# Performance work log

Hardware: AMD Instinct MI355X
Metric: run time of the kernel (lower is better)

The kernel has to match this reference:

```python
import jax, jax.numpy as jnp
from jax import lax
import numpy as np

DN = ('NCHW', 'OIHW', 'NCHW')


def conv(x, w, b, pad=0):
    y = lax.conv_general_dilated(x, w, (1, 1), [(pad, pad), (pad, pad)],
                                 dimension_numbers=DN)
    return y + b[None, :, None, None]


def deconv(x, w, b, stride=1):
    # PyTorch ConvTranspose2d weight is (in, out, kH, kW); equivalent conv uses
    # flipped, in/out-transposed kernel with lhs dilation = stride, pad = k-1.
    k = w.shape[2]
    wt = jnp.flip(w, (2, 3)).transpose(1, 0, 2, 3)
    y = lax.conv_general_dilated(x, wt, (1, 1), [(k - 1, k - 1), (k - 1, k - 1)],
                                 lhs_dilation=(stride, stride), dimension_numbers=DN)
    return y + b[None, :, None, None]


def maxpool2(x):
    return lax.reduce_window(x, -jnp.inf, lax.max, (1, 1, 2, 2), (1, 1, 2, 2), 'VALID')


def setup_inputs() -> dict:
    key = jax.random.key(0)
    ks = jax.random.split(key, 12)
    B = 256

    def he(k, shape, fan_in):
        return jax.random.normal(k, shape, jnp.float32) * np.sqrt(2.0 / fan_in)

    inp = {
        'x': jax.random.normal(ks[0], (B, 1, 28, 28), jnp.float32),
        # encoder convs
        'w1': he(ks[1], (128, 1, 5, 5), 1 * 25), 'b1': jnp.zeros((128,), jnp.float32),
        'w2': he(ks[2], (128, 128, 5, 5), 128 * 25), 'b2': jnp.zeros((128,), jnp.float32),
        'w3': he(ks[3], (128, 128, 5, 5), 128 * 25), 'b3': jnp.zeros((128,), jnp.float32),
        # decoder transposed convs (torch shape: in, out, kH, kW)
        't1w': he(ks[4], (128, 128, 4, 4), 128 * 16), 't1b': jnp.zeros((128,), jnp.float32),
        't2w': he(ks[5], (128, 128, 4, 4), 128 * 16), 't2b': jnp.zeros((128,), jnp.float32),
        't3w': he(ks[6], (128, 128, 5, 5), 128 * 25), 't3b': jnp.zeros((128,), jnp.float32),
        't4w': he(ks[7], (128, 128, 5, 5), 128 * 25), 't4b': jnp.zeros((128,), jnp.float32),
        # mu_net 1x1 conv
        'mw': he(ks[8], (1, 128, 1, 1), 128), 'mb': jnp.zeros((1,), jnp.float32),
        # codebook: Embedding(128, 128), init ~ N(0, 1)
        'dict_w': jax.random.normal(ks[9], (128, 128), jnp.float32),
    }
    return inp


def reference(x, w1, b1, w2, b2, w3, b3,
              t1w, t1b, t2w, t2b, t3w, t3b, t4w, t4b,
              mw, mb, dict_w):
    BETA, RATE = 0.25, 5.0
    # ---- encoder ----
    h = jax.nn.relu(conv(x, w1, b1, pad=0))          # (B,128,24,24)
    h = jax.nn.relu(conv(h, w2, b2, pad=2))          # (B,128,24,24)
    h = maxpool2(h)                                  # (B,128,12,12)
    h = conv(h, w3, b3, pad=2)                       # (B,128,12,12)
    z = maxpool2(h)                                  # (B,128,6,6)

    # ---- nearest_neighbor (faithful: argmax of distance, as in the source) ----
    z_sg = lax.stop_gradient(z)
    z2 = jnp.sum(z_sg * z_sg, axis=1, keepdims=True)          # (B,1,6,6)
    w2n = jnp.sum(dict_w * dict_w, axis=1)                     # (K,)
    cross = jnp.einsum('bchw,kc->bkhw', z_sg, lax.stop_gradient(dict_w))
    d2 = z2 + w2n[None, :, None, None] - 2.0 * cross           # (B,K,6,6)
    index = jnp.argmax(d2, axis=1)                             # (B,6,6) int

    # ---- embedding gather ----
    val = dict_w[index].transpose(0, 3, 1, 2)                  # (B,128,6,6)

    # ---- decoder on detached codes ----
    f = lax.stop_gradient(val)
    f = jax.nn.relu(deconv(f, t1w, t1b, stride=1))             # (B,128,9,9)
    f = jax.nn.relu(deconv(f, t2w, t2b, stride=2))             # (B,128,20,20)
    f = jax.nn.relu(deconv(f, t3w, t3b, stride=1))             # (B,128,24,24)
    f = jax.nn.relu(deconv(f, t4w, t4b, stride=1))             # (B,128,28,28)
    mu = conv(f, mw, mb, pad=0)                                # (B,1,28,28)

    loss_rec = jnp.mean((mu - x) ** 2)
    dict_loss = jnp.mean((val - lax.stop_gradient(z)) ** 2) * RATE
    enc_loss = jnp.mean((z - lax.stop_gradient(val)) ** 2) * BETA * RATE
    var_loss = jnp.zeros((), jnp.float32)
    losses = jnp.stack([loss_rec, dict_loss, enc_loss, var_loss])
    return losses, index
```

## Files before the change

kernel.cpp:

```cpp
#include <hip/hip_runtime.h>
#include <hip/hip_bf16.h>


#define B_ 256

typedef __attribute__((ext_vector_type(8))) short s16x8;
typedef __attribute__((ext_vector_type(4))) short s16x4;
typedef __attribute__((ext_vector_type(8))) _Float16 f16x8;
typedef __attribute__((ext_vector_type(4))) float f32x4;

__device__ inline ushort f2bf(float f) {
  union { __hip_bfloat16 h; ushort u; } cv;
  cv.h = __float2bfloat16(f);
  return cv.u;
}

__global__ __launch_bounds__(256) void prep_all(
    const float* __restrict__ t1w, const float* __restrict__ t3w,
    const float* __restrict__ t4w, const float* __restrict__ t2w,
    const float* __restrict__ w2, const float* __restrict__ w3,
    ushort* __restrict__ wp1, ushort* __restrict__ wp3,
    ushort* __restrict__ wp4, ushort* __restrict__ wp2,
    _Float16* __restrict__ w2h, _Float16* __restrict__ w2l,
    _Float16* __restrict__ w3h, _Float16* __restrict__ w3l) {
  const int b = blockIdx.x, t = threadIdx.x;
  if (b < 1024) {
    int idx = b * 256 + t;
    int ci = idx & 127, co = (idx >> 7) & 127, tap = idx >> 14;
    wp1[idx] = f2bf(t1w[((size_t)ci * 128 + co) * 16 + (15 - tap)]);
  } else if (b < 2624) {
    int idx = (b - 1024) * 256 + t;
    int ci = idx & 127, co = (idx >> 7) & 127, tap = idx >> 14;
    wp3[idx] = f2bf(t3w[((size_t)ci * 128 + co) * 25 + (24 - tap)]);
  } else if (b < 4224) {
    int idx = (b - 2624) * 256 + t;
    int ci = idx & 127, co = (idx >> 7) & 127, tap = idx >> 14;
    wp4[idx] = f2bf(t4w[((size_t)ci * 128 + co) * 25 + (24 - tap)]);
  } else if (b < 5248) {
    int idx = (b - 4224) * 256 + t;
    int ci = idx & 127, co = (idx >> 7) & 127;
    int tap = (idx >> 14) & 3, pp = idx >> 16;
    int u = tap >> 1, v = tap & 1, py = pp >> 1, px = pp & 1;
    wp2[idx] = f2bf(
        t2w[(((size_t)ci * 128 + co) * 4 + (py + 2 * u)) * 4 + (px + 2 * v)]);
  } else if (b < 6848) {
    int idx = (b - 5248) * 256 + t;
    int ci = idx & 127, co = (idx >> 7) & 127, tap = idx >> 14;
    float v = w2[((size_t)co * 128 + ci) * 25 + tap];
    _Float16 h = (_Float16)v;
    w2h[idx] = h;
    w2l[idx] = (_Float16)(v - (float)h);
  } else {
    int idx = (b - 6848) * 256 + t;
    int ci = idx & 127, co = (idx >> 7) & 127, tap = idx >> 14;
    float v = w3[((size_t)co * 128 + ci) * 25 + tap];
    _Float16 h = (_Float16)v;
    w3h[idx] = h;
    w3l[idx] = (_Float16)(v - (float)h);
  }
}

__global__ __launch_bounds__(256) void conv1_kernel(
    const float* __restrict__ x, const float* __restrict__ w,
    const float* __restrict__ b, _Float16* __restrict__ oh,
    _Float16* __restrict__ ol) {
  const int n = blockIdx.x;
  __shared__ float xl[784];
  __shared__ float wl[128 * 25];
  __shared__ float bl[128];
  const int t = threadIdx.x;
  for (int e = t; e < 784; e += 256) xl[e] = x[n * 784 + e];
  for (int e = t; e < 3200; e += 256) wl[e] = w[e];
  if (t < 128) bl[t] = b[t];
  __syncthreads();
  const size_t nb = (size_t)n * 73728;
  for (int idx = t; idx < 73728; idx += 256) {
    int co = idx & 127, p = idx >> 7;
    int y = p / 24, xx = p % 24;
    float acc = bl[co];
    const float* wc = &wl[co * 25];
#pragma unroll
    for (int ky = 0; ky < 5; ky++)
#pragma unroll
      for (int kx = 0; kx < 5; kx++)
        acc += xl[(y + ky) * 28 + xx + kx] * wc[ky * 5 + kx];
    float v = fmaxf(acc, 0.f);
    _Float16 h = (_Float16)v;
    oh[nb + idx] = h;
    ol[nb + idx] = (_Float16)(v - (float)h);
  }
}

template <int IW, int K, int PAD, int TR, bool RELU, bool OUT_F32, int PWX>
__global__ __launch_bounds__(256, 3) void conv_mfma_pool(
    const _Float16* __restrict__ inh, const _Float16* __restrict__ inl,
    const _Float16* __restrict__ wph, const _Float16* __restrict__ wpl,
    const float* __restrict__ bias, _Float16* __restrict__ outh,
    _Float16* __restrict__ outl, float* __restrict__ outf) {
  constexpr int IH = IW, OW = IW, OH = IW;
  constexpr int PW = PWX;
  constexpr int SROWS = TR + K - 1;
  constexpr int S = SROWS * PW;
  constexpr int NPOS = TR * OW;
  constexpr int NCH = NPOS / 16;
  constexpr int SCRP = NPOS + 1;
  constexpr int K2 = K * K;
  constexpr int PITCH = 40;
  constexpr int LIN_ELT = S * PITCH;
  constexpr int LIN_BYTES = 2 * LIN_ELT * 2;
  constexpr int SCR_BYTES = 64 * SCRP * 4;
  constexpr int SMEM_BYTES = LIN_BYTES > SCR_BYTES ? LIN_BYTES : SCR_BYTES;
  static_assert(NPOS % 16 == 0, "");
  static_assert(TR % 2 == 0 && OW % 2 == 0, "");
  static_assert(PW >= OW + K - 1, "");
  __shared__ __align__(16) char smem[SMEM_BYTES];
  _Float16* linh = (_Float16*)smem;
  _Float16* linl = linh + LIN_ELT;
  const int n = blockIdx.x;
  const int r0 = blockIdx.y * TR;
  const int t = threadIdx.x;
  const int wv = t >> 6;
  const int lane = t & 63;
  const int nn = lane & 15;
  const int q = lane >> 4;
  f32x4 acc0[NCH], acc1[NCH];
  int boff[NCH];
#pragma unroll
  for (int c = 0; c < NCH; c++) {
    acc0[c] = f32x4{0.f, 0.f, 0.f, 0.f};
    acc1[c] = f32x4{0.f, 0.f, 0.f, 0.f};
    int p = c * 16 + nn;
    boff[c] = ((p / OW) * PW + (p % OW)) * PITCH + q * 8;
  }
  const int rowA = wv * 16 + nn;
  const int rowB = (wv + 4) * 16 + nn;
  for (int cb = 0; cb < 4; cb++) {
    const int ci0 = cb * 32;
    __syncthreads();
    for (int e = t; e < S * 4; e += 256) {
      int sp = e >> 2, j = e & 3;
      int r = sp / PW, c = sp - r * PW;
      int ir = r0 + r - PAD, ic = c - PAD;
      f16x8 vh = {0, 0, 0, 0, 0, 0, 0, 0};
      f16x8 vl = {0, 0, 0, 0, 0, 0, 0, 0};
      if (ir >= 0 && ir < IH && ic >= 0 && ic < IW) {
        size_t g = ((size_t)n * (IH * IW) + ir * IW + ic) * 128 + ci0 + j * 8;
        vh = *(const f16x8*)&inh[g];
        vl = *(const f16x8*)&inl[g];
      }
      int st = sp * PITCH + j * 8;
      *(f16x8*)&linh[st] = vh;
      *(f16x8*)&linl[st] = vl;
    }
    __syncthreads();
    const size_t gA = (size_t)rowA * 128 + ci0 + q * 8;
    const size_t gB = (size_t)rowB * 128 + ci0 + q * 8;
    f16x8 cah0 = *(const f16x8*)&wph[gA];
    f16x8 cal0 = *(const f16x8*)&wpl[gA];
    f16x8 cah1 = *(const f16x8*)&wph[gB];
    f16x8 cal1 = *(const f16x8*)&wpl[gB];
    for (int tap = 0; tap < K2; tap++) {
      f16x8 nah0 = cah0, nal0 = cal0, nah1 = cah1, nal1 = cal1;
      if (tap + 1 < K2) {
        size_t oA = gA + (size_t)(tap + 1) * 16384;
        size_t oB = gB + (size_t)(tap + 1) * 16384;
        nah0 = *(const f16x8*)&wph[oA];
        nal0 = *(const f16x8*)&wpl[oA];
        nah1 = *(const f16x8*)&wph[oB];
        nal1 = *(const f16x8*)&wpl[oB];
      }
      const int ky = tap / K, kx = tap - ky * K;
      const int tp = (ky * PW + kx) * PITCH;
#pragma unroll
      for (int c = 0; c < NCH; c++) {
        int off = boff[c] + tp;
        f16x8 bh = *(const f16x8*)&linh[off];
        f16x8 bl = *(const f16x8*)&linl[off];
        acc0[c] =
            __builtin_amdgcn_mfma_f32_16x16x32_f16(cah0, bh, acc0[c], 0, 0, 0);
        acc0[c] =
            __builtin_amdgcn_mfma_f32_16x16x32_f16(cah0, bl, acc0[c], 0, 0, 0);
        acc0[c] =
            __builtin_amdgcn_mfma_f32_16x16x32_f16(cal0, bh, acc0[c], 0, 0, 0);
        acc1[c] =
            __builtin_amdgcn_mfma_f32_16x16x32_f16(cah1, bh, acc1[c], 0, 0, 0);
        acc1[c] =
            __builtin_amdgcn_mfma_f32_16x16x32_f16(cah1, bl, acc1[c], 0, 0, 0);
        acc1[c] =
            __builtin_amdgcn_mfma_f32_16x16x32_f16(cal1, bh, acc1[c], 0, 0, 0);
      }
      cah0 = nah0; cal0 = nal0; cah1 = nah1; cal1 = nal1;
    }
  }
  __syncthreads();
  float* scr = (float*)smem + wv * 16 * SCRP;
#pragma unroll
  for (int j = 0; j < 2; j++) {
    const int cot = (j ? wv + 4 : wv) * 16;
#pragma unroll
    for (int c = 0; c < NCH; c++) {
      f32x4 a = j ? acc1[c] : acc0[c];
#pragma unroll
      for (int r = 0; r < 4; r++) {
        float v = a[r] + bias[cot + q * 4 + r];
        if (RELU) v = fmaxf(v, 0.f);
        scr[(q * 4 + r) * SCRP + c * 16 + nn] = v;
      }
    }
    __syncthreads();
    for (int e = lane; e < 16 * (TR / 2) * (OW / 2); e += 64) {
      int co_l = e & 15;
      int rem = e >> 4;
      int pr = rem / (OW / 2), pc = rem - pr * (OW / 2);
      const float* s = scr + co_l * SCRP;
      int lp = (2 * pr) * OW + 2 * pc;
      float m =
          fmaxf(fmaxf(s[lp], s[lp + 1]), fmaxf(s[lp + OW], s[lp + OW + 1]));
      int sp_out = (r0 / 2 + pr) * (OW / 2) + pc;
      size_t go =
          ((size_t)n * ((OH / 2) * (OW / 2)) + sp_out) * 128 + cot + co_l;
      if (OUT_F32) {
        outf[go] = m;
      } else {
        _Float16 h = (_Float16)m;
        outh[go] = h;
        outl[go] = (_Float16)(m - (float)h);
      }
    }
    __syncthreads();
  }
}

__global__ __launch_bounds__(256) void vq_kernel(
    const float* __restrict__ z, const float* __restrict__ dict,
    float* __restrict__ val, ushort* __restrict__ val_bf,
    float* __restrict__ out_idx) {
  const int n = blockIdx.x;
  __shared__ float zl[36 * 128];
  __shared__ float d2[36 * 129];
  __shared__ float w2n[128];
  __shared__ int bk[36];
  const int t = threadIdx.x;
  const float* zn = z + (size_t)n * 4608;
  for (int e = t; e < 4608; e += 256) zl[e] = zn[e];
  if (t < 128) {
    float s = 0.f;
    const float* wr = dict + t * 128;
    for (int c = 0; c < 128; c++) s += wr[c] * wr[c];
    w2n[t] = s;
  }
  __syncthreads();
  const int k = t & 127, pg = t >> 7;
  float dot[18];
#pragma unroll
  for (int i = 0; i < 18; i++) dot[i] = 0.f;
  const float* wr = dict + k * 128;
  for (int c = 0; c < 128; c++) {
    float wv = wr[c];
#pragma unroll
    for (int i = 0; i < 18; i++) dot[i] += zl[(pg * 18 + i) * 128 + c] * wv;
  }
  float wn = w2n[k];
#pragma unroll
  for (int i = 0; i < 18; i++) d2[(pg * 18 + i) * 129 + k] = wn - 2.f * dot[i];
  __syncthreads();
  if (t < 36) {
    const float* dr = &d2[t * 129];
    float best = dr[0];
    int bi = 0;
    for (int kk = 1; kk < 128; kk++) {
      float v = dr[kk];
      if (v > best) { best = v; bi = kk; }
    }
    bk[t] = bi;
    out_idx[n * 36 + t] = (float)bi;
  }
  __syncthreads();
  float* vn = val + (size_t)n * 4608;
  ushort* vbn = val_bf + (size_t)n * 4608;
  for (int e = t; e < 4608; e += 256) {
    int c = e & 127, p = e >> 7;
    float v = dict[bk[p] * 128 + c];
    vn[e] = v;
    vbn[e] = f2bf(v);
  }
}

template <int IH, int IW, int OH, int OW, int K, int TR, bool MU_FUSE, int PWX>
__global__ __launch_bounds__(256, 2) void deconv_mfma(
    const ushort* __restrict__ in, const ushort* __restrict__ wprep,
    const float* __restrict__ bias, const float* __restrict__ mw,
    void* __restrict__ outp) {
  constexpr int PAD = K - 1;
  constexpr int PW = PWX;
  constexpr int K2 = K * K;
  constexpr int SROWS = TR + K - 1;
  constexpr int S = SROWS * PW;
  constexpr int NPOS = TR * OW;
  constexpr int NCH = (NPOS + 15) / 16;
  constexpr int PITCH = 40;
  constexpr int LIN_ELT = S * PITCH;
  constexpr int NSTG = (S * 4 + 255) / 256;
  static_assert(PW >= OW + K - 1, "");
  __shared__ __align__(16) ushort lin[2][LIN_ELT];
  const int n = blockIdx.x;
  const int r0 = blockIdx.y * TR;
  const int t = threadIdx.x;
  const int wv = t >> 6;
  const int lane = t & 63;
  const int nn = lane & 15;
  const int q = lane >> 4;
  f32x4 acc0[NCH], acc1[NCH];
  int boff[NCH];
#pragma unroll
  for (int c = 0; c < NCH; c++) {
    acc0[c] = f32x4{0.f, 0.f, 0.f, 0.f};
    acc1[c] = f32x4{0.f, 0.f, 0.f, 0.f};
    int p = c * 16 + nn;
    int pc = p < NPOS ? p : NPOS - 1;
    boff[c] = ((pc / OW) * PW + (pc % OW)) * PITCH + q * 8;
  }
  s16x8 stg[NSTG];
  auto load_stage = [&](int ci0) {
#pragma unroll
    for (int i = 0; i < NSTG; i++) {
      int e = t + i * 256;
      s16x8 v = {0, 0, 0, 0, 0, 0, 0, 0};
      if (e < S * 4) {
        int sp = e >> 2, j = e & 3;
        int rr = sp / PW, cc = sp - rr * PW;
        int ir = r0 + rr - PAD, ic = cc - PAD;
        if (ir >= 0 && ir < IH && ic >= 0 && ic < IW)
          v = *(const s16x8*)&in[((size_t)n * (IH * IW) + ir * IW + ic) * 128 +
                                 ci0 + j * 8];
      }
      stg[i] = v;
    }
  };
  auto store_stage = [&](int bsel) {
#pragma unroll
    for (int i = 0; i < NSTG; i++) {
      int e = t + i * 256;
      if (e < S * 4) {
        int sp = e >> 2, j = e & 3;
        *(s16x8*)&lin[bsel][sp * PITCH + j * 8] = stg[i];
      }
    }
  };

  load_stage(0);
  store_stage(0);
  __syncthreads();
  for (int cb = 0; cb < 4; cb++) {
    const int ci0 = cb * 32;
    if (cb < 3) load_stage(ci0 + 32);
    const ushort* L = lin[cb & 1];
    const size_t gA = (size_t)(wv * 16 + nn) * 128 + ci0 + q * 8;
    const size_t gB = (size_t)((wv + 4) * 16 + nn) * 128 + ci0 + q * 8;
    s16x8 ca0 = *(const s16x8*)&wprep[gA];
    s16x8 ca1 = *(const s16x8*)&wprep[gB];
    for (int tap = 0; tap < K2; tap++) {
      s16x8 na0 = ca0, na1 = ca1;
      if (tap + 1 < K2) {
        na0 = *(const s16x8*)&wprep[gA + (size_t)(tap + 1) * 16384];
        na1 = *(const s16x8*)&wprep[gB + (size_t)(tap + 1) * 16384];
      }
      const int ky = tap / K, kx = tap - ky * K;
      const int tp = (ky * PW + kx) * PITCH;
#pragma unroll
      for (int c = 0; c < NCH; c++) {
        s16x8 b = *(const s16x8*)&L[boff[c] + tp];
        acc0[c] =
            __builtin_amdgcn_mfma_f32_16x16x32_bf16(ca0, b, acc0[c], 0, 0, 0);
        acc1[c] =
            __builtin_amdgcn_mfma_f32_16x16x32_bf16(ca1, b, acc1[c], 0, 0, 0);
      }
      ca0 = na0; ca1 = na1;
    }
    if (cb < 3) {
      store_stage((cb + 1) & 1);
      __syncthreads();
    }
  }
  const int co_a = wv * 16 + q * 4;
  const int co_b = (wv + 4) * 16 + q * 4;
  float ba[4], bb[4];
#pragma unroll
  for (int r = 0; r < 4; r++) {
    ba[r] = bias[co_a + r];
    bb[r] = bias[co_b + r];
  }
  if (!MU_FUSE) {
    ushort* out = (ushort*)outp;
#pragma unroll
    for (int c = 0; c < NCH; c++) {
      int p = c * 16 + nn;
      if (p < NPOS) {
        size_t go = ((size_t)n * (OH * OW) + r0 * OW + p) * 128;
        s16x4 pa, pb;
#pragma unroll
        for (int r = 0; r < 4; r++) {
          pa[r] = (short)f2bf(fmaxf(acc0[c][r] + ba[r], 0.f));
          pb[r] = (short)f2bf(fmaxf(acc1[c][r] + bb[r], 0.f));
        }
        *(s16x4*)&out[go + co_a] = pa;
        *(s16x4*)&out[go + co_b] = pb;
      }
    }
  } else {
    float* out = (float*)outp;
    float wa[4], wb[4];
#pragma unroll
    for (int r = 0; r < 4; r++) {
      wa[r] = mw[co_a + r];
      wb[r] = mw[co_b + r];
    }
#pragma unroll
    for (int c = 0; c < NCH; c++) {
      int p = c * 16 + nn;
      float s = 0.f;
#pragma unroll
      for (int r = 0; r < 4; r++) {
        s += fmaxf(acc0[c][r] + ba[r], 0.f) * wa[r];
        s += fmaxf(acc1[c][r] + bb[r], 0.f) * wb[r];
      }
      s += __shfl_xor(s, 16);
      s += __shfl_xor(s, 32);
      if (q == 0 && p < NPOS)
        atomicAdd(&out[(size_t)n * (OH * OW) + r0 * OW + p], s);
    }
  }
}

__global__ __launch_bounds__(256, 3) void deconv_s2_mfma(
    const ushort* __restrict__ in, const ushort* __restrict__ wp2,
    const float* __restrict__ bias, ushort* __restrict__ out) {
  constexpr int NCH = 7;
  constexpr int PITCH = 40;
  constexpr int PW = 18;
  constexpr int S = 11 * PW;
  const int n = blockIdx.x;
  const int pp = blockIdx.y;
  const int py = pp >> 1, px = pp & 1;
  __shared__ __align__(16) ushort lin[S * PITCH];
  const int t = threadIdx.x;
  const int wv = t >> 6;
  const int lane = t & 63;
  const int nn = lane & 15;
  const int q = lane >> 4;
  f32x4 acc0[NCH], acc1[NCH];
  int boff[NCH];
#pragma unroll
  for (int c = 0; c < NCH; c++) {
    acc0[c] = f32x4{0.f, 0.f, 0.f, 0.f};
    acc1[c] = f32x4{0.f, 0.f, 0.f, 0.f};
    int p = c * 16 + nn;
    int pc = p < 100 ? p : 99;
    boff[c] = ((pc / 10) * PW + (pc % 10)) * PITCH + q * 8;
  }
  const int toffs[4] = {PW + 1, PW, 1, 0};
  for (int cb = 0; cb < 4; cb++) {
    const int ci0 = cb * 32;
    __syncthreads();
    for (int e = t; e < S * 4; e += 256) {
      int sp = e >> 2, j = e & 3;
      int r = sp / PW, c2 = sp - r * PW;
      int ir = r - 1, ic = c2 - 1;
      s16x8 v = {0, 0, 0, 0, 0, 0, 0, 0};
      if (ir >= 0 && ir < 9 && ic >= 0 && ic < 9)
        v = *(const s16x8*)&in[((size_t)n * 81 + ir * 9 + ic) * 128 + ci0 +
                               j * 8];
      *(s16x8*)&lin[sp * PITCH + j * 8] = v;
    }
    __syncthreads();
    const size_t gA =
        ((size_t)(pp * 4) * 128 + wv * 16 + nn) * 128 + ci0 + q * 8;
    const size_t gB =
        ((size_t)(pp * 4) * 128 + (wv + 4) * 16 + nn) * 128 + ci0 + q * 8;
    s16x8 ca0 = *(const s16x8*)&wp2[gA];
    s16x8 ca1 = *(const s16x8*)&wp2[gB];
    for (int tap = 0; tap < 4; tap++) {
      s16x8 na0 = ca0, na1 = ca1;
      if (tap + 1 < 4) {
        na0 = *(const s16x8*)&wp2[gA + (size_t)(tap + 1) * 16384];
        na1 = *(const s16x8*)&wp2[gB + (size_t)(tap + 1) * 16384];
      }
      const int tp = toffs[tap] * PITCH;
#pragma unroll
      for (int c = 0; c < NCH; c++) {
        s16x8 b = *(const s16x8*)&lin[boff[c] + tp];
        acc0[c] =
            __builtin_amdgcn_mfma_f32_16x16x32_bf16(ca0, b, acc0[c], 0, 0, 0);
        acc1[c] =
            __builtin_amdgcn_mfma_f32_16x16x32_bf16(ca1, b, acc1[c], 0, 0, 0);
      }
      ca0 = na0; ca1 = na1;
    }
  }
  const int co_a = wv * 16 + q * 4;
  const int co_b = (wv + 4) * 16 + q * 4;
#pragma unroll
  for (int c = 0; c < NCH; c++) {
    int p = c * 16 + nn;
    if (p < 100) {
      int oy = 2 * (p / 10) + py, ox = 2 * (p % 10) + px;
      size_t go = ((size_t)n * 400 + oy * 20 + ox) * 128;
      s16x4 pa, pb;
#pragma unroll
      for (int r = 0; r < 4; r++) {
        pa[r] = (short)f2bf(fmaxf(acc0[c][r] + bias[co_a + r], 0.f));
        pb[r] = (short)f2bf(fmaxf(acc1[c][r] + bias[co_b + r], 0.f));
      }
      *(s16x4*)&out[go + co_a] = pa;
      *(s16x4*)&out[go + co_b] = pb;
    }
  }
}

__global__ __launch_bounds__(256) void loss_kernel(
    const float* __restrict__ mu, const float* __restrict__ mb,
    const float* __restrict__ x, const float4* __restrict__ val4,
    const float4* __restrict__ z4, float* __restrict__ out) {
  const int b = blockIdx.x, t = threadIdx.x;
  __shared__ float red[256];
  if (b < 784) {
    int i = b * 256 + t;
    float d = mu[i] + mb[0] - x[i];
    red[t] = d * d;
  } else {
    int i = (b - 784) * 256 + t;
    float4 a = val4[i], zz = z4[i];
    float dx = a.x - zz.x, dy = a.y - zz.y, dz = a.z - zz.z, dw = a.w - zz.w;
    red[t] = dx * dx + dy * dy + dz * dz + dw * dw;
  }
  __syncthreads();
  for (int off = 128; off > 0; off >>= 1) {
    if (t < off) red[t] += red[t + off];
    __syncthreads();
  }
  if (t == 0) {
    if (b < 784) {
      atomicAdd(out, red[0] * (1.0f / 200704.f));
    } else {
      atomicAdd(out + 1, red[0] * (5.f / 1179648.f));
      atomicAdd(out + 2, red[0] * (1.25f / 1179648.f));
    }
  }
}

extern "C" void kernel_launch(void* const* d_in, const int* in_sizes, int n_in,
                              void* d_out, int out_size, void* d_ws,
                              size_t ws_size, hipStream_t stream) {
  const float* x = (const float*)d_in[0];
  const float* w1 = (const float*)d_in[1];
  const float* b1 = (const float*)d_in[2];
  const float* w2 = (const float*)d_in[3];
  const float* b2 = (const float*)d_in[4];
  const float* w3 = (const float*)d_in[5];
  const float* b3 = (const float*)d_in[6];
  const float* t1w = (const float*)d_in[7];
  const float* t1b = (const float*)d_in[8];
  const float* t2w = (const float*)d_in[9];
  const float* t2b = (const float*)d_in[10];
  const float* t3w = (const float*)d_in[11];
  const float* t3b = (const float*)d_in[12];
  const float* t4w = (const float*)d_in[13];
  const float* t4b = (const float*)d_in[14];
  const float* mw = (const float*)d_in[15];
  const float* mb = (const float*)d_in[16];
  const float* dictw = (const float*)d_in[17];
  float* out = (float*)d_out;

  float* p = (float*)d_ws;
  _Float16* h1h = (_Float16*)p; p += 9437184;
  _Float16* h1l = (_Float16*)p; p += 9437184;
  _Float16* p1h = (_Float16*)p; p += 2359296;
  _Float16* p1l = (_Float16*)p; p += 2359296;
  float* z = p; p += 1179648;
  float* val = p; p += 1179648;
  ushort* val_bf = (ushort*)p; p += 589824;
  float* mu = p; p += 200704;
  ushort* wp1 = (ushort*)p; p += 131072;
  ushort* wp3 = (ushort*)p; p += 204800;
  ushort* wp4 = (ushort*)p; p += 204800;
  ushort* wp2 = (ushort*)p; p += 131072;
  _Float16* w2h = (_Float16*)p; p += 204800;
  _Float16* w2l = (_Float16*)p; p += 204800;
  _Float16* w3h = (_Float16*)p; p += 204800;
  _Float16* w3l = (_Float16*)p; p += 204800;
  ushort* f1 = (ushort*)p1h;
  ushort* f2 = (ushort*)h1l;
  ushort* f3 = (ushort*)h1h;

  hipMemsetAsync(d_out, 0, 4 * sizeof(float), stream);
  hipMemsetAsync(mu, 0, 200704 * sizeof(float), stream);

  prep_all<<<8448, 256, 0, stream>>>(t1w, t3w, t4w, t2w, w2, w3, wp1, wp3, wp4,
                                     wp2, w2h, w2l, w3h, w3l);

  conv1_kernel<<<B_, 256, 0, stream>>>(x, w1, b1, h1h, h1l);
  conv_mfma_pool<24, 5, 2, 6, true, false, 28>
      <<<dim3(B_, 4), 256, 0, stream>>>(h1h, h1l, w2h, w2l, b2, p1h, p1l,
                                        nullptr);
  conv_mfma_pool<12, 5, 2, 4, false, true, 20>
      <<<dim3(B_, 3), 256, 0, stream>>>(p1h, p1l, w3h, w3l, b3, nullptr,
                                        nullptr, z);
  vq_kernel<<<B_, 256, 0, stream>>>(z, dictw, val, val_bf, out + 4);
  deconv_mfma<6, 6, 9, 9, 4, 9, false, 17>
      <<<dim3(B_, 1), 256, 0, stream>>>(val_bf, wp1, t1b, nullptr, f1);
  deconv_s2_mfma<<<dim3(B_, 4), 256, 0, stream>>>(f1, wp2, t2b, f2);
  deconv_mfma<20, 20, 24, 24, 5, 8, false, 28>
      <<<dim3(B_, 3), 256, 0, stream>>>(f2, wp3, t3b, nullptr, f3);
  deconv_mfma<24, 24, 28, 28, 5, 7, true, 36>
      <<<dim3(B_, 4), 256, 0, stream>>>(f3, wp4, t4b, mw, mu);
  loss_kernel<<<1936, 256, 0, stream>>>(mu, mb, x, (const float4*)val,
                                        (const float4*)z, out);
}
```

Measured before the change: 913.3 us.

## Specialize conv2 with register-blocked MFMA tiles and double-buffered weight prefetch

Replaces the generic templated conv2+pool kernel with a dedicated kernel. Each wave holds a 5x4 block of 16x16 accumulators, covering 64 output channels by up to 80 positions, so each LDS B-fragment feeds four MFMA groups. Weight fragments for the next tap are prefetched from global into registers, and the next channel chunk of input is staged through registers while the current one computes. The larger accumulator footprint lowers occupancy to two blocks per CU, and the pooling epilogue runs in four passes through a shared scratch buffer.

```diff
diff --git a/kernel.cpp b/kernel.cpp
--- a/kernel.cpp
+++ b/kernel.cpp
@@ -91,6 +91,164 @@
   }
 }
 
+__global__ __launch_bounds__(256, 2) void conv2_mfma_pool(
+    const _Float16* __restrict__ inh, const _Float16* __restrict__ inl,
+    const _Float16* __restrict__ wph, const _Float16* __restrict__ wpl,
+    const float* __restrict__ bias, _Float16* __restrict__ outh,
+    _Float16* __restrict__ outl) {
+  constexpr int PW = 28;
+  constexpr int S = 10 * PW;
+  constexpr int NPOS = 144;
+  constexpr int SCRP = NPOS + 1;
+  constexpr int PITCH = 40;
+  constexpr int LIN_ELT = S * PITCH;
+  __shared__ __align__(16) char smem[2 * LIN_ELT * 2];
+  _Float16* linh = (_Float16*)smem;
+  _Float16* linl = linh + LIN_ELT;
+  const int n = blockIdx.x;
+  const int r0 = blockIdx.y * 6;
+  const int t = threadIdx.x;
+  const int wv = t >> 6;
+  const int lane = t & 63;
+  const int nn = lane & 15;
+  const int q = lane >> 4;
+  const int pairid = wv >> 1;
+  const int coset = wv & 1;
+  f32x4 acc[5][4];
+#pragma unroll
+  for (int cL = 0; cL < 5; cL++)
+#pragma unroll
+    for (int g = 0; g < 4; g++) acc[cL][g] = f32x4{0.f, 0.f, 0.f, 0.f};
+  int boff[5];
+#pragma unroll
+  for (int cL = 0; cL < 5; cL++) {
+    int cg = pairid ? 5 + cL : cL;
+    int p = cg * 16 + nn;
+    boff[cL] = ((p / 24) * PW + (p % 24)) * PITCH + q * 8;
+  }
+  size_t gA[4];
+#pragma unroll
+  for (int g = 0; g < 4; g++)
+    gA[g] = (size_t)(coset * 64 + g * 16 + nn) * 128 + q * 8;
+
+  f16x8 stgh[5], stgl[5];
+  auto load_stage = [&](int ci0) {
+#pragma unroll
+    for (int i = 0; i < 5; i++) {
+      int e = t + i * 256;
+      f16x8 vh = {0, 0, 0, 0, 0, 0, 0, 0};
+      f16x8 vl = {0, 0, 0, 0, 0, 0, 0, 0};
+      if (e < S * 4) {
+        int sp = e >> 2, j = e & 3;
+        int r = sp / PW, c = sp - r * PW;
+        int ir = r0 + r - 2, ic = c - 2;
+        if (ir >= 0 && ir < 24 && ic >= 0 && ic < 24) {
+          size_t g2 = ((size_t)n * 576 + ir * 24 + ic) * 128 + ci0 + j * 8;
+          vh = *(const f16x8*)&inh[g2];
+          vl = *(const f16x8*)&inl[g2];
+        }
+      }
+      stgh[i] = vh;
+      stgl[i] = vl;
+    }
+  };
+  auto store_stage = [&]() {
+#pragma unroll
+    for (int i = 0; i < 5; i++) {
+      int e = t + i * 256;
+      if (e < S * 4) {
+        int sp = e >> 2, j = e & 3;
+        *(f16x8*)&linh[sp * PITCH + j * 8] = stgh[i];
+        *(f16x8*)&linl[sp * PITCH + j * 8] = stgl[i];
+      }
+    }
+  };
+
+  load_stage(0);
+  store_stage();
+  __syncthreads();
+  for (int cb = 0; cb < 4; cb++) {
+    const int ci0 = cb * 32;
+    f16x8 cah[4], cal[4];
+#pragma unroll
+    for (int g = 0; g < 4; g++) {
+      cah[g] = *(const f16x8*)&wph[gA[g] + ci0];
+      cal[g] = *(const f16x8*)&wpl[gA[g] + ci0];
+    }
+    if (cb < 3) load_stage(ci0 + 32);
+    for (int tap = 0; tap < 25; tap++) {
+      f16x8 nah[4], nal[4];
+#pragma unroll
+      for (int g = 0; g < 4; g++) { nah[g] = cah[g]; nal[g] = cal[g]; }
+      if (tap + 1 < 25) {
+        const size_t to = (size_t)(tap + 1) * 16384 + ci0;
+#pragma unroll
+        for (int g = 0; g < 4; g++) {
+          nah[g] = *(const f16x8*)&wph[gA[g] + to];
+          nal[g] = *(const f16x8*)&wpl[gA[g] + to];
+        }
+      }
+      const int ky = tap / 5, kx = tap - ky * 5;
+      const int tp = (ky * PW + kx) * PITCH;
+#pragma unroll
+      for (int cL = 0; cL < 5; cL++) {
+        if (pairid == 0 || cL < 4) {
+          f16x8 bh = *(const f16x8*)&linh[boff[cL] + tp];
+          f16x8 bl = *(const f16x8*)&linl[boff[cL] + tp];
+#pragma unroll
+          for (int g = 0; g < 4; g++) {
+            acc[cL][g] = __builtin_amdgcn_mfma_f32_16x16x32_f16(cah[g], bh,
+                                                               acc[cL][g], 0, 0, 0);
+            acc[cL][g] = __builtin_amdgcn_mfma_f32_16x16x32_f16(cah[g], bl,
+                                                               acc[cL][g], 0, 0, 0);
+            acc[cL][g] = __builtin_amdgcn_mfma_f32_16x16x32_f16(cal[g], bh,
+                                                               acc[cL][g], 0, 0, 0);
+          }
+        }
+      }
+#pragma unroll
+      for (int g = 0; g < 4; g++) { cah[g] = nah[g]; cal[g] = nal[g]; }
+    }
+    if (cb < 3) {
+      __syncthreads();
+      store_stage();
+      __syncthreads();
+    }
+  }
+  __syncthreads();
+  float* scr = (float*)smem;
+#pragma unroll
+  for (int g = 0; g < 4; g++) {
+#pragma unroll
+    for (int cL = 0; cL < 5; cL++) {
+      if (pairid == 0 || cL < 4) {
+        const int cg = pairid ? 5 + cL : cL;
+#pragma unroll
+        for (int r = 0; r < 4; r++) {
+          float v =
+              fmaxf(acc[cL][g][r] + bias[coset * 64 + g * 16 + q * 4 + r], 0.f);
+          scr[(coset * 16 + q * 4 + r) * SCRP + cg * 16 + nn] = v;
+        }
+      }
+    }
+    __syncthreads();
+    for (int e = t; e < 1152; e += 256) {
+      int co32 = e & 31, rem = e >> 5;
+      int pr = rem / 12, pc = rem - pr * 12;
+      const float* s = scr + co32 * SCRP;
+      int lp = (2 * pr) * 24 + 2 * pc;
+      float m =
+          fmaxf(fmaxf(s[lp], s[lp + 1]), fmaxf(s[lp + 24], s[lp + 25]));
+      int co_g = (co32 >> 4) * 64 + g * 16 + (co32 & 15);
+      size_t go = ((size_t)n * 144 + (size_t)(r0 / 2 + pr) * 12 + pc) * 128 + co_g;
+      _Float16 h = (_Float16)m;
+      outh[go] = h;
+      outl[go] = (_Float16)(m - (float)h);
+    }
+    __syncthreads();
+  }
+}
+
 template <int IW, int K, int PAD, int TR, bool RELU, bool OUT_F32, int PWX>
 __global__ __launch_bounds__(256, 3) void conv_mfma_pool(
     const _Float16* __restrict__ inh, const _Float16* __restrict__ inl,
@@ -599,9 +757,8 @@
                                      wp2, w2h, w2l, w3h, w3l);
 
   conv1_kernel<<<B_, 256, 0, stream>>>(x, w1, b1, h1h, h1l);
-  conv_mfma_pool<24, 5, 2, 6, true, false, 28>
-      <<<dim3(B_, 4), 256, 0, stream>>>(h1h, h1l, w2h, w2l, b2, p1h, p1l,
-                                        nullptr);
+  conv2_mfma_pool<<<dim3(B_, 4), 256, 0, stream>>>(h1h, h1l, w2h, w2l, b2,
+                                                   p1h, p1l);
   conv_mfma_pool<12, 5, 2, 4, false, true, 20>
       <<<dim3(B_, 3), 256, 0, stream>>>(p1h, p1l, w3h, w3l, b3, nullptr,
                                         nullptr, z);
```

Result: slower. 1.014 ms (+11.0%).

## Retile deconv MFMA warps into 64-channel by half-position tiles

Applied to the files above, without the earlier changes.

Each wave previously computed 32 output channels (two 16-row groups) across all position tiles. Now wave pairs split the position tiles and each wave covers 64 output channels (four groups), so each LDS B-fragment load feeds four MFMAs instead of two. This cuts LDS read traffic per MFMA, but each wave now issues twice as many weight loads per tap. The uneven split when NCH is odd also leaves the second pair of waves with less work.

```diff
diff --git a/kernel.cpp b/kernel.cpp
--- a/kernel.cpp
+++ b/kernel.cpp
@@ -287,7 +287,8 @@
 }
 
 template <int IH, int IW, int OH, int OW, int K, int TR, bool MU_FUSE, int PWX>
-__global__ __launch_bounds__(256, 2) void deconv_mfma(
+__global__ __attribute__((amdgpu_flat_work_group_size(256, 256),
+                          amdgpu_waves_per_eu(2, 2))) void deconv_mfma(
     const ushort* __restrict__ in, const ushort* __restrict__ wprep,
     const float* __restrict__ bias, const float* __restrict__ mw,
     void* __restrict__ outp) {
@@ -298,6 +299,8 @@
   constexpr int S = SROWS * PW;
   constexpr int NPOS = TR * OW;
   constexpr int NCH = (NPOS + 15) / 16;
+  constexpr int NT0 = (NCH + 1) / 2;
+  constexpr int NT1 = NCH - NT0;
   constexpr int PITCH = 40;
   constexpr int LIN_ELT = S * PITCH;
   constexpr int NSTG = (S * 4 + 255) / 256;
@@ -310,15 +313,19 @@
   const int lane = t & 63;
   const int nn = lane & 15;
   const int q = lane >> 4;
-  f32x4 acc0[NCH], acc1[NCH];
-  int boff[NCH];
-#pragma unroll
-  for (int c = 0; c < NCH; c++) {
-    acc0[c] = f32x4{0.f, 0.f, 0.f, 0.f};
-    acc1[c] = f32x4{0.f, 0.f, 0.f, 0.f};
-    int p = c * 16 + nn;
+  const int pairid = wv >> 1;
+  const int cohalf = wv & 1;
+  f32x4 acc[NT0][4];
+  int boff[NT0];
+#pragma unroll
+  for (int tL = 0; tL < NT0; tL++) {
+#pragma unroll
+    for (int g = 0; g < 4; g++) acc[tL][g] = f32x4{0.f, 0.f, 0.f, 0.f};
+    int tg = pairid * NT0 + tL;
+    if (tg > NCH - 1) tg = NCH - 1;
+    int p = tg * 16 + nn;
     int pc = p < NPOS ? p : NPOS - 1;
-    boff[c] = ((pc / OW) * PW + (pc % OW)) * PITCH + q * 8;
+    boff[tL] = ((pc / OW) * PW + (pc % OW)) * PITCH + q * 8;
   }
   s16x8 stg[NSTG];
   auto load_stage = [&](int ci0) {
@@ -355,79 +362,95 @@
     const int ci0 = cb * 32;
     if (cb < 3) load_stage(ci0 + 32);
     const ushort* L = lin[cb & 1];
-    const size_t gA = (size_t)(wv * 16 + nn) * 128 + ci0 + q * 8;
-    const size_t gB = (size_t)((wv + 4) * 16 + nn) * 128 + ci0 + q * 8;
-    s16x8 ca0 = *(const s16x8*)&wprep[gA];
-    s16x8 ca1 = *(const s16x8*)&wprep[gB];
+    size_t gA[4];
+#pragma unroll
+    for (int g = 0; g < 4; g++)
+      gA[g] = (size_t)(cohalf * 64 + g * 16 + nn) * 128 + ci0 + q * 8;
+    s16x8 ca[4];
+#pragma unroll
+    for (int g = 0; g < 4; g++) ca[g] = *(const s16x8*)&wprep[gA[g]];
     for (int tap = 0; tap < K2; tap++) {
-      s16x8 na0 = ca0, na1 = ca1;
+      s16x8 na[4];
+#pragma unroll
+      for (int g = 0; g < 4; g++) na[g] = ca[g];
       if (tap + 1 < K2) {
-        na0 = *(const s16x8*)&wprep[gA + (size_t)(tap + 1) * 16384];
-        na1 = *(const s16x8*)&wprep[gB + (size_t)(tap + 1) * 16384];
+        const size_t to = (size_t)(tap + 1) * 16384;
+#pragma unroll
+        for (int g = 0; g < 4; g++)
+          na[g] = *(const s16x8*)&wprep[gA[g] + to];
       }
       const int ky = tap / K, kx = tap - ky * K;
       const int tp = (ky * PW + kx) * PITCH;
 #pragma unroll
-      for (int c = 0; c < NCH; c++) {
-        s16x8 b = *(const s16x8*)&L[boff[c] + tp];
-        acc0[c] =
-            __builtin_amdgcn_mfma_f32_16x16x32_bf16(ca0, b, acc0[c], 0, 0, 0);
-        acc1[c] =
-            __builtin_amdgcn_mfma_f32_16x16x32_bf16(ca1, b, acc1[c], 0, 0, 0);
-      }
-      ca0 = na0; ca1 = na1;
+      for (int tL = 0; tL < NT0; tL++) {
+        if (pairid == 0 || tL < NT1) {
+          s16x8 b = *(const s16x8*)&L[boff[tL] + tp];
+#pragma unroll
+          for (int g = 0; g < 4; g++)
+            acc[tL][g] = __builtin_amdgcn_mfma_f32_16x16x32_bf16(ca[g], b,
+                                                                acc[tL][g], 0,
+                                                                0, 0);
+        }
+      }
+#pragma unroll
+      for (int g = 0; g < 4; g++) ca[g] = na[g];
     }
     if (cb < 3) {
       store_stage((cb + 1) & 1);
       __syncthreads();
     }
   }
-  const int co_a = wv * 16 + q * 4;
-  const int co_b = (wv + 4) * 16 + q * 4;
-  float ba[4], bb[4];
-#pragma unroll
-  for (int r = 0; r < 4; r++) {
-    ba[r] = bias[co_a + r];
-    bb[r] = bias[co_b + r];
-  }
+  float bav[4][4];
+#pragma unroll
+  for (int g = 0; g < 4; g++)
+#pragma unroll
+    for (int r = 0; r < 4; r++)
+      bav[g][r] = bias[cohalf * 64 + g * 16 + q * 4 + r];
   if (!MU_FUSE) {
     ushort* out = (ushort*)outp;
 #pragma unroll
-    for (int c = 0; c < NCH; c++) {
-      int p = c * 16 + nn;
-      if (p < NPOS) {
-        size_t go = ((size_t)n * (OH * OW) + r0 * OW + p) * 128;
-        s16x4 pa, pb;
-#pragma unroll
-        for (int r = 0; r < 4; r++) {
-          pa[r] = (short)f2bf(fmaxf(acc0[c][r] + ba[r], 0.f));
-          pb[r] = (short)f2bf(fmaxf(acc1[c][r] + bb[r], 0.f));
+    for (int tL = 0; tL < NT0; tL++) {
+      if (pairid == 0 || tL < NT1) {
+        int tg = pairid * NT0 + tL;
+        int p = tg * 16 + nn;
+        if (p < NPOS) {
+          size_t go =
+              ((size_t)n * (OH * OW) + r0 * OW + p) * 128 + cohalf * 64;
+#pragma unroll
+          for (int g = 0; g < 4; g++) {
+            s16x4 pk;
+#pragma unroll
+            for (int r = 0; r < 4; r++)
+              pk[r] = (short)f2bf(fmaxf(acc[tL][g][r] + bav[g][r], 0.f));
+            *(s16x4*)&out[go + g * 16 + q * 4] = pk;
+          }
         }
-        *(s16x4*)&out[go + co_a] = pa;
-        *(s16x4*)&out[go + co_b] = pb;
       }
     }
   } else {
     float* out = (float*)outp;
-    float wa[4], wb[4];
-#pragma unroll
-    for (int r = 0; r < 4; r++) {
-      wa[r] = mw[co_a + r];
-      wb[r] = mw[co_b + r];
-    }
-#pragma unroll
-    for (int c = 0; c < NCH; c++) {
-      int p = c * 16 + nn;
-      float s = 0.f;
-#pragma unroll
-      for (int r = 0; r < 4; r++) {
-        s += fmaxf(acc0[c][r] + ba[r], 0.f) * wa[r];
-        s += fmaxf(acc1[c][r] + bb[r], 0.f) * wb[r];
-      }
-      s += __shfl_xor(s, 16);
-      s += __shfl_xor(s, 32);
-      if (q == 0 && p < NPOS)
-        atomicAdd(&out[(size_t)n * (OH * OW) + r0 * OW + p], s);
+    float mwv[4][4];
+#pragma unroll
+    for (int g = 0; g < 4; g++)
+#pragma unroll
+      for (int r = 0; r < 4; r++)
+        mwv[g][r] = mw[cohalf * 64 + g * 16 + q * 4 + r];
+#pragma unroll
+    for (int tL = 0; tL < NT0; tL++) {
+      if (pairid == 0 || tL < NT1) {
+        int tg = pairid * NT0 + tL;
+        int p = tg * 16 + nn;
+        float s = 0.f;
+#pragma unroll
+        for (int g = 0; g < 4; g++)
+#pragma unroll
+          for (int r = 0; r < 4; r++)
+            s += fmaxf(acc[tL][g][r] + bav[g][r], 0.f) * mwv[g][r];
+        s += __shfl_xor(s, 16);
+        s += __shfl_xor(s, 32);
+        if (q == 0 && p < NPOS)
+          atomicAdd(&out[(size_t)n * (OH * OW) + r0 * OW + p], s);
+      }
     }
   }
 }
```

Result: slower. 1.031 ms (+12.9%).
